# Kernel tuning notes

Hardware: AMD Instinct MI355X
Metric: run time of the kernel (lower is better)

The kernel has to match this reference:

```python
import jax, jax.numpy as jnp
import numpy as np

# Model constants (match init_kwargs)
DIM = 256
H = 8
HD = DIM // H          # 32
WIN = 5                # spatial window_size
QS = 4                 # quant_size
CQS = 2 * QS           # color_quant_size = 8
CWIN = 2               # color_windowsize
W = 64                 # voxels per window (equal-size windows for the reference)
L_XYZ = WIN * QS       # 20 -> table length 40
L_RGB = CWIN * CQS     # 16 -> table length 32


def setup_inputs() -> dict:
    key = jax.random.key(0)
    ks = jax.random.split(key, 12)
    N = 8192
    feats = jax.random.normal(ks[0], (N, DIM), dtype=jnp.float32)
    xyz = jax.random.uniform(ks[1], (N, 3), dtype=jnp.float32) * WIN    # [0, window_size)
    rgb = jax.random.uniform(ks[2], (N, 3), dtype=jnp.float32) * CWIN   # [0, color_windowsize)
    n_coords = jnp.concatenate([xyz, rgb], axis=1)
    std = 0.02
    xyz_shape = (3, 2 * L_XYZ, H, HD)
    rgb_shape = (3, 2 * L_RGB, H, HD)
    return {
        "feats": feats,
        "n_coords": n_coords,
        "qkv_w": jax.random.normal(ks[3], (3 * DIM, DIM), dtype=jnp.float32) * std,
        "qkv_b": jnp.zeros((3 * DIM,), dtype=jnp.float32),
        "q_xyz_t": jax.random.normal(ks[4], xyz_shape, dtype=jnp.float32) * std,
        "k_xyz_t": jax.random.normal(ks[5], xyz_shape, dtype=jnp.float32) * std,
        "v_xyz_t": jax.random.normal(ks[6], xyz_shape, dtype=jnp.float32) * std,
        "q_rgb_t": jax.random.normal(ks[7], rgb_shape, dtype=jnp.float32) * std,
        "k_rgb_t": jax.random.normal(ks[8], rgb_shape, dtype=jnp.float32) * std,
        "v_rgb_t": jax.random.normal(ks[9], rgb_shape, dtype=jnp.float32) * std,
        "proj_w": jax.random.normal(ks[10], (DIM, DIM), dtype=jnp.float32) * std,
        "proj_b": jnp.zeros((DIM,), dtype=jnp.float32),
    }


def _attn_bias(q, k, idx, q_table, k_table):
    """Relative-signal bias added to QK logits.
    q,k: [nw, W, H, hd]; idx: [nw, W, W, 3] int; tables: [3, T, H, hd].
    bias[n,h,i,j] = sum_c q[n,i,h]. q_table[c, idx[n,i,j,c], h] + k[n,j,h]. k_table[c, idx, h]
    Returns (bias [nw,H,W,W], one_hot [nw,W,W,3,T]) so the one-hot is reused for the value bias.
    """
    T = q_table.shape[1]
    oh = jax.nn.one_hot(idx, T, dtype=q.dtype)                # [nw,W,W,3,T]
    dq = jnp.einsum('nihd,cthd->nicht', q, q_table)           # per-voxel dot vs all table rows
    dk = jnp.einsum('njhd,cthd->njcht', k, k_table)
    bias_q = jnp.einsum('nicht,nijct->nhij', dq, oh)
    bias_k = jnp.einsum('njcht,nijct->nhij', dk, oh)
    return bias_q + bias_k, oh


def _value_bias(attn, oh, v_table):
    """out[n,i,h,:] += sum_j attn[n,h,i,j] * sum_c v_table[c, idx[n,i,j,c], h, :]"""
    at = jnp.einsum('nhij,nijct->nhict', attn, oh)            # scatter attn mass onto table rows
    return jnp.einsum('nhict,cthd->nihd', at, v_table)


def reference(feats, n_coords, qkv_w, qkv_b, q_xyz_t, k_xyz_t, v_xyz_t,
              q_rgb_t, k_rgb_t, v_rgb_t, proj_w, proj_b):
    N = feats.shape[0]
    nw = N // W
    scale = HD ** (-0.5)

    # QKV projection, split into per-window heads
    qkv = (feats @ qkv_w.T + qkv_b).reshape(nw, W, 3, H, HD)
    q = qkv[:, :, 0] * scale
    k = qkv[:, :, 1]
    v = qkv[:, :, 2]

    # Quantized relative-signal indices (coordinate deltas, offset to [0, 2L))
    scaled = jnp.concatenate(
        [n_coords[:, 0:3] * QS, n_coords[:, 3:6] * CQS], axis=1)   # [N, 6]
    cw = scaled.reshape(nw, W, 6)
    delta = jnp.floor(cw[:, :, None, :] - cw[:, None, :, :]).astype(jnp.int32)
    offs = jnp.array([L_XYZ] * 3 + [L_RGB] * 3, dtype=jnp.int32)
    hi = jnp.array([2 * L_XYZ - 1] * 3 + [2 * L_RGB - 1] * 3, dtype=jnp.int32)
    idx = jnp.clip(delta + offs, 0, hi)                        # [nw, W, W, 6]
    idx_xyz, idx_rgb = idx[..., :3], idx[..., 3:]

    bias_x, oh_x = _attn_bias(q, k, idx_xyz, q_xyz_t, k_xyz_t)
    bias_r, oh_r = _attn_bias(q, k, idx_rgb, q_rgb_t, k_rgb_t)

    logits = jnp.einsum('nihd,njhd->nhij', q, k) + bias_x + bias_r
    attn = jax.nn.softmax(logits, axis=-1)

    out = (jnp.einsum('nhij,njhd->nihd', attn, v)
           + _value_bias(attn, oh_x, v_xyz_t)
           + _value_bias(attn, oh_r, v_rgb_t))
    out = out.reshape(N, DIM)
    return out @ proj_w.T + proj_b
```

## Files before the change

kernel.cpp:

```cpp
#include <hip/hip_runtime.h>


typedef __attribute__((ext_vector_type(8))) short short8;
typedef __attribute__((ext_vector_type(4))) float f32x4;

__device__ __forceinline__ unsigned short f2bf(float f) {
    union { float f; unsigned int u; } v; v.f = f;
    unsigned int r = v.u + 0x7FFFu + ((v.u >> 16) & 1u);
    return (unsigned short)(r >> 16);
}

#define LFENCE() asm volatile("s_waitcnt lgkmcnt(0)" ::: "memory")

__global__ __launch_bounds__(256) void k_cast(
    const float* __restrict__ feats, const float* __restrict__ qkvw,
    const float* __restrict__ pw,
    ushort* __restrict__ fb, ushort* __restrict__ qwb, ushort* __restrict__ pwb)
{
    int t = blockIdx.x * 256 + threadIdx.x;
    const float* src; ushort* dst; int off;
    if (t < 262144)            { src = feats; dst = fb;  off = t; }
    else if (t < 286720)       { src = qkvw;  dst = qwb; off = t - 262144; }
    else                       { src = pw;    dst = pwb; off = t - 286720; }
    const float* s = src + (size_t)off * 8;
    float4 v0 = *(const float4*)s, v1 = *(const float4*)(s + 4);
    union { ushort u[8]; uint4 v; } pk;
    pk.u[0] = f2bf(v0.x); pk.u[1] = f2bf(v0.y); pk.u[2] = f2bf(v0.z); pk.u[3] = f2bf(v0.w);
    pk.u[4] = f2bf(v1.x); pk.u[5] = f2bf(v1.y); pk.u[6] = f2bf(v1.z); pk.u[7] = f2bf(v1.w);
    *(uint4*)(dst + (size_t)off * 8) = pk.v;
}

__global__ __launch_bounds__(256) void k_qkv(
    const ushort* __restrict__ A, const ushort* __restrict__ B,
    const float* __restrict__ bias,
    ushort* __restrict__ qb, ushort* __restrict__ kb, ushort* __restrict__ vb)
{
    __shared__ __align__(16) ushort a_s[64 * 72];
    __shared__ __align__(16) ushort b_s[64 * 72];
    const int tid = threadIdx.x;
    const int m0 = blockIdx.y * 64;
    const int n0 = blockIdx.x * 64;
    const int w = tid >> 6, wm = w >> 1, wn = w & 1;
    const int l4 = tid & 15, quad = (tid >> 4) & 3;
    f32x4 acc[2][2];
#pragma unroll
    for (int mt = 0; mt < 2; ++mt)
#pragma unroll
        for (int nt = 0; nt < 2; ++nt) acc[mt][nt] = (f32x4){0.f, 0.f, 0.f, 0.f};

    for (int k0 = 0; k0 < 256; k0 += 64) {
#pragma unroll
        for (int l = 0; l < 2; ++l) {
            int e = tid + l * 256;
            int row = e >> 3, kq = e & 7;
            *(uint4*)&a_s[row * 72 + kq * 8] =
                *(const uint4*)(A + (size_t)(m0 + row) * 256 + k0 + kq * 8);
            *(uint4*)&b_s[row * 72 + kq * 8] =
                *(const uint4*)(B + (size_t)(n0 + row) * 256 + k0 + kq * 8);
        }
        __syncthreads();
#pragma unroll
        for (int kh = 0; kh < 2; ++kh) {
            short8 bf0 = *(const short8*)&b_s[(wn * 32 + l4) * 72 + kh * 32 + quad * 8];
            short8 bf1 = *(const short8*)&b_s[(wn * 32 + 16 + l4) * 72 + kh * 32 + quad * 8];
#pragma unroll
            for (int mt = 0; mt < 2; ++mt) {
                short8 af = *(const short8*)&a_s[(wm * 32 + mt * 16 + l4) * 72 + kh * 32 + quad * 8];
                acc[mt][0] = __builtin_amdgcn_mfma_f32_16x16x32_bf16(af, bf0, acc[mt][0], 0, 0, 0);
                acc[mt][1] = __builtin_amdgcn_mfma_f32_16x16x32_bf16(af, bf1, acc[mt][1], 0, 0, 0);
            }
        }
        __syncthreads();
    }
#pragma unroll
    for (int nt = 0; nt < 2; ++nt) {
        int c = n0 + wn * 32 + nt * 16 + l4;
        float bv = bias[c];
        int s = c >> 8, rem = c & 255, h = rem >> 5, d = rem & 31;
        ushort* dst = (s == 0) ? qb : ((s == 1) ? kb : vb);
        float mul = (s == 0) ? 0.17677669529663687f : 1.0f;
#pragma unroll
        for (int mt = 0; mt < 2; ++mt) {
            int mbase = m0 + wm * 32 + mt * 16 + quad * 4;
#pragma unroll
            for (int reg = 0; reg < 4; ++reg) {
                int m = mbase + reg;
                int nw = m >> 6, ii = m & 63;
                dst[((size_t)((nw * 8 + h) * 64 + ii)) * 32 + d] = f2bf((acc[mt][nt][reg] + bv) * mul);
            }
        }
    }
}

#define DBS 44
#define FXS 16777216.0f
#define FXI (1.0f / 16777216.0f)

__global__ __launch_bounds__(256, 2) void k_bias(
    const ushort* __restrict__ qb, const ushort* __restrict__ kb,
    const float* __restrict__ nco,
    const float* __restrict__ kxt, const float* __restrict__ krt,
    float* __restrict__ lgt)
{
    __shared__ __align__(16) float dbuf[64 * DBS];
    __shared__ __align__(16) ushort q_s[64 * 40];
    __shared__ __align__(16) ushort k_s[64 * 40];
    __shared__ __align__(16) ushort tbl[128 * 40];
    __shared__ __align__(16) float cwf[64 * 6];

    const int tid = threadIdx.x;
    const int n = blockIdx.x >> 3;
    const int h = blockIdx.x & 7;
    const int w = tid >> 6;
    const int l4 = tid & 15;
    const int quad = (tid >> 4) & 3;

    const size_t base = (size_t)((n * 8 + h) * 64) * 32;

    {
        int row = tid >> 2, part = tid & 3;
        *(uint4*)&q_s[row * 40 + part * 8] = *(const uint4*)(qb + base + tid * 8);
        *(uint4*)&k_s[row * 40 + part * 8] = *(const uint4*)(kb + base + tid * 8);
    }
    if (tid < 64) {
        const float* cp = nco + (size_t)(n * 64 + tid) * 6;
        cwf[tid * 6 + 0] = cp[0] * 4.f; cwf[tid * 6 + 1] = cp[1] * 4.f;
        cwf[tid * 6 + 2] = cp[2] * 4.f; cwf[tid * 6 + 3] = cp[3] * 8.f;
        cwf[tid * 6 + 4] = cp[4] * 8.f; cwf[tid * 6 + 5] = cp[5] * 8.f;
    }

    auto stageTbl = [&](const float* tbg, int R, int Rpad) {
        for (int e = tid; e < R * 4; e += 256) {
            int r = e >> 2, part = e & 3;
            const float* src = tbg + (size_t)r * 256 + part * 8;
            float4 f0 = *(const float4*)src, f1 = *(const float4*)(src + 4);
            union { ushort u[8]; uint4 v; } pk;
            pk.u[0] = f2bf(f0.x); pk.u[1] = f2bf(f0.y); pk.u[2] = f2bf(f0.z); pk.u[3] = f2bf(f0.w);
            pk.u[4] = f2bf(f1.x); pk.u[5] = f2bf(f1.y); pk.u[6] = f2bf(f1.z); pk.u[7] = f2bf(f1.w);
            *(uint4*)&tbl[r * 40 + part * 8] = pk.v;
        }
        for (int e = tid; e < (Rpad - R) * 40; e += 256) tbl[R * 40 + e] = 0;
    };

    float lg[4][4];
    int ibase[4];
#pragma unroll
    for (int r = 0; r < 4; ++r) ibase[r] = (w * 16 + quad * 4 + r) * DBS;

    auto tgemmC = [&](const ushort* a_s, int c, int T) {
        short8 af = *(const short8*)&a_s[(w * 16 + l4) * 40 + quad * 8];
        const int NT = (T == 40) ? 3 : 2;
        for (int tt = 0; tt < NT; ++tt) {
            short8 bf = *(const short8*)&tbl[(c * T + tt * 16 + l4) * 40 + quad * 8];
            f32x4 a = {0.f, 0.f, 0.f, 0.f};
            a = __builtin_amdgcn_mfma_f32_16x16x32_bf16(af, bf, a, 0, 0, 0);
            int col = tt * 16 + l4;
            int rb = w * 16 + quad * 4;
            if (col < T) {
                dbuf[(rb + 0) * DBS + col] = a[0];
                dbuf[(rb + 1) * DBS + col] = a[1];
                dbuf[(rb + 2) * DBS + col] = a[2];
                dbuf[(rb + 3) * DBS + col] = a[3];
            }
        }
    };

    stageTbl(kxt + h * 32, 120, 128);
    __syncthreads();

    unsigned idxp[24];
    {
        float co[4][6], cl[4][6];
#pragma unroll
        for (int r = 0; r < 4; ++r) {
            int j = w * 16 + quad * 4 + r;
#pragma unroll
            for (int c6 = 0; c6 < 6; ++c6) co[r][c6] = cwf[j * 6 + c6];
        }
#pragma unroll
        for (int tt = 0; tt < 4; ++tt) {
            int i = tt * 16 + l4;
#pragma unroll
            for (int c6 = 0; c6 < 6; ++c6) cl[tt][c6] = cwf[i * 6 + c6];
        }
#pragma unroll
        for (int c6 = 0; c6 < 6; ++c6) {
            const int off = (c6 < 3) ? 20 : 16, hi = (c6 < 3) ? 39 : 31;
#pragma unroll
            for (int tt = 0; tt < 4; ++tt) {
                unsigned p = 0;
#pragma unroll
                for (int r = 0; r < 4; ++r) {
                    int x = min(max((int)floorf(cl[tt][c6] - co[r][c6]) + off, 0), hi);
                    p |= (unsigned)x << (8 * r);
                }
                idxp[c6 * 4 + tt] = p;
            }
        }
    }

    auto gatherT = [&](int cc) {
#pragma unroll
        for (int tt = 0; tt < 4; ++tt) {
            unsigned p = idxp[cc * 4 + tt];
#pragma unroll
            for (int r = 0; r < 4; ++r) {
                int x = (p >> (8 * r)) & 255;
                lg[tt][r] += dbuf[ibase[r] + x];
            }
        }
    };

    {
        short8 ak = *(const short8*)&k_s[(w * 16 + l4) * 40 + quad * 8];
#pragma unroll
        for (int tt = 0; tt < 4; ++tt) {
            short8 bq = *(const short8*)&q_s[(tt * 16 + l4) * 40 + quad * 8];
            f32x4 r = {0.f, 0.f, 0.f, 0.f};
            r = __builtin_amdgcn_mfma_f32_16x16x32_bf16(ak, bq, r, 0, 0, 0);
            lg[tt][0] = r[0]; lg[tt][1] = r[1]; lg[tt][2] = r[2]; lg[tt][3] = r[3];
        }
    }

    tgemmC(k_s, 0, 40); LFENCE();
    gatherT(0); LFENCE();
    tgemmC(k_s, 1, 40); LFENCE();
    gatherT(1); LFENCE();
    tgemmC(k_s, 2, 40); LFENCE();
    gatherT(2);
    __syncthreads();
    stageTbl(krt + h * 32, 96, 96);
    __syncthreads();
    tgemmC(k_s, 0, 32); LFENCE();
    gatherT(3); LFENCE();
    tgemmC(k_s, 1, 32); LFENCE();
    gatherT(4); LFENCE();
    tgemmC(k_s, 2, 32); LFENCE();
    gatherT(5);

    {
        float* lp = lgt + (size_t)(n * 8 + h) * 4096;
#pragma unroll
        for (int tt = 0; tt < 4; ++tt)
#pragma unroll
            for (int reg = 0; reg < 4; ++reg)
                lp[(w * 16 + quad * 4 + reg) * 64 + tt * 16 + l4] = lg[tt][reg];
    }
}

__global__ __launch_bounds__(256, 2) void k_av(
    const ushort* __restrict__ qb, const ushort* __restrict__ vb,
    const float* __restrict__ nco,
    const float* __restrict__ qxt, const float* __restrict__ vxt,
    const float* __restrict__ qrt, const float* __restrict__ vrt,
    const float* __restrict__ lgt,
    ushort* __restrict__ aout)
{
    __shared__ __align__(16) float dbuf[64 * DBS];
    __shared__ __align__(16) ushort U[11264];
    __shared__ __align__(16) float cwf[64 * 6];
    ushort* q_s  = U;
    ushort* tbl  = U + 2560;
    ushort* attn_s = U;
    ushort* v_t    = U + 4608;
    ushort* vtbl   = U + 6912;

    const int tid = threadIdx.x;
    const int n = blockIdx.x >> 3;
    const int h = blockIdx.x & 7;
    const int w = tid >> 6;
    const int lane = tid & 63;
    const int l4 = tid & 15;
    const int quad = (tid >> 4) & 3;

    const size_t base = (size_t)((n * 8 + h) * 64) * 32;

    {
        int row = tid >> 2, part = tid & 3;
        *(uint4*)&q_s[row * 40 + part * 8] = *(const uint4*)(qb + base + tid * 8);
    }
    if (tid < 64) {
        const float* cp = nco + (size_t)(n * 64 + tid) * 6;
        cwf[tid * 6 + 0] = cp[0] * 4.f; cwf[tid * 6 + 1] = cp[1] * 4.f;
        cwf[tid * 6 + 2] = cp[2] * 4.f; cwf[tid * 6 + 3] = cp[3] * 8.f;
        cwf[tid * 6 + 4] = cp[4] * 8.f; cwf[tid * 6 + 5] = cp[5] * 8.f;
    }

    auto stageTbl = [&](const float* tbg, int R, int Rpad) {
        for (int e = tid; e < R * 4; e += 256) {
            int r = e >> 2, part = e & 3;
            const float* src = tbg + (size_t)r * 256 + part * 8;
            float4 f0 = *(const float4*)src, f1 = *(const float4*)(src + 4);
            union { ushort u[8]; uint4 v; } pk;
            pk.u[0] = f2bf(f0.x); pk.u[1] = f2bf(f0.y); pk.u[2] = f2bf(f0.z); pk.u[3] = f2bf(f0.w);
            pk.u[4] = f2bf(f1.x); pk.u[5] = f2bf(f1.y); pk.u[6] = f2bf(f1.z); pk.u[7] = f2bf(f1.w);
            *(uint4*)&tbl[r * 40 + part * 8] = pk.v;
        }
        for (int e = tid; e < (Rpad - R) * 40; e += 256) tbl[R * 40 + e] = 0;
    };
    auto stageVtbl = [&](const float* tbg, int R) {
        for (int e = tid; e < R * 4; e += 256) {
            int r = e >> 2, part = e & 3;
            const float* src = tbg + (size_t)r * 256 + part * 8;
            float4 f0 = *(const float4*)src, f1 = *(const float4*)(src + 4);
            int d0 = part * 8;
            vtbl[(d0 + 0) * 136 + r] = f2bf(f0.x);
            vtbl[(d0 + 1) * 136 + r] = f2bf(f0.y);
            vtbl[(d0 + 2) * 136 + r] = f2bf(f0.z);
            vtbl[(d0 + 3) * 136 + r] = f2bf(f0.w);
            vtbl[(d0 + 4) * 136 + r] = f2bf(f1.x);
            vtbl[(d0 + 5) * 136 + r] = f2bf(f1.y);
            vtbl[(d0 + 6) * 136 + r] = f2bf(f1.z);
            vtbl[(d0 + 7) * 136 + r] = f2bf(f1.w);
        }
    };
    auto stageVt = [&]() {
        int j = tid >> 2, d0 = (tid & 3) * 8;
        uint4 pk = *(const uint4*)(vb + base + tid * 8);
        const ushort* u = (const ushort*)&pk;
#pragma unroll
        for (int ii = 0; ii < 8; ++ii) v_t[(d0 + ii) * 72 + j] = u[ii];
    };

    float lg[4][4];
    {
        const float* lp = lgt + (size_t)(n * 8 + h) * 4096;
        int i0 = w * 16 + quad * 4;
#pragma unroll
        for (int tt = 0; tt < 4; ++tt) {
            f32x4 v = *(const f32x4*)(lp + (size_t)(tt * 16 + l4) * 64 + i0);
            lg[tt][0] = v[0]; lg[tt][1] = v[1]; lg[tt][2] = v[2]; lg[tt][3] = v[3];
        }
    }

    int ibase[4];
#pragma unroll
    for (int r = 0; r < 4; ++r) ibase[r] = (w * 16 + quad * 4 + r) * DBS;

    auto tgemmC = [&](const ushort* a_s, int c, int T) {
        short8 af = *(const short8*)&a_s[(w * 16 + l4) * 40 + quad * 8];
        const int NT = (T == 40) ? 3 : 2;
        for (int tt = 0; tt < NT; ++tt) {
            short8 bf = *(const short8*)&tbl[(c * T + tt * 16 + l4) * 40 + quad * 8];
            f32x4 a = {0.f, 0.f, 0.f, 0.f};
            a = __builtin_amdgcn_mfma_f32_16x16x32_bf16(af, bf, a, 0, 0, 0);
            int col = tt * 16 + l4;
            int rb = w * 16 + quad * 4;
            if (col < T) {
                dbuf[(rb + 0) * DBS + col] = a[0];
                dbuf[(rb + 1) * DBS + col] = a[1];
                dbuf[(rb + 2) * DBS + col] = a[2];
                dbuf[(rb + 3) * DBS + col] = a[3];
            }
        }
    };
    auto zeroOwn = [&]() {
        float4 z = {0.f, 0.f, 0.f, 0.f};
        float4* rb = (float4*)&dbuf[w * 16 * DBS];
        for (int v = lane; v < 176; v += 64) rb[v] = z;
    };

    stageTbl(qxt + h * 32, 120, 128);
    __syncthreads();

    unsigned idxp[24];
    {
        float co[4][6], cl[4][6];
#pragma unroll
        for (int r = 0; r < 4; ++r) {
            int i = w * 16 + quad * 4 + r;
#pragma unroll
            for (int c6 = 0; c6 < 6; ++c6) co[r][c6] = cwf[i * 6 + c6];
        }
#pragma unroll
        for (int tt = 0; tt < 4; ++tt) {
            int j = tt * 16 + l4;
#pragma unroll
            for (int c6 = 0; c6 < 6; ++c6) cl[tt][c6] = cwf[j * 6 + c6];
        }
#pragma unroll
        for (int c6 = 0; c6 < 6; ++c6) {
            const int off = (c6 < 3) ? 20 : 16, hi = (c6 < 3) ? 39 : 31;
#pragma unroll
            for (int tt = 0; tt < 4; ++tt) {
                unsigned p = 0;
#pragma unroll
                for (int r = 0; r < 4; ++r) {
                    int x = min(max((int)floorf(co[r][c6] - cl[tt][c6]) + off, 0), hi);
                    p |= (unsigned)x << (8 * r);
                }
                idxp[c6 * 4 + tt] = p;
            }
        }
    }

    auto gatherC = [&](int cc) {
#pragma unroll
        for (int tt = 0; tt < 4; ++tt) {
            unsigned p = idxp[cc * 4 + tt];
#pragma unroll
            for (int r = 0; r < 4; ++r) {
                int x = (p >> (8 * r)) & 255;
                lg[tt][r] += dbuf[ibase[r] + x];
            }
        }
    };
    auto scatterC = [&](int cc) {
        unsigned* bb = (unsigned*)dbuf;
#pragma unroll
        for (int tt = 0; tt < 4; ++tt) {
            unsigned p = idxp[cc * 4 + tt];
#pragma unroll
            for (int r = 0; r < 4; ++r) {
                int x = (p >> (8 * r)) & 255;
                unsigned q = (unsigned)(lg[tt][r] * FXS + 0.5f);
                atomicAdd(&bb[ibase[r] + x], q);
            }
        }
    };

    tgemmC(q_s, 0, 40); LFENCE();
    gatherC(0); LFENCE();
    tgemmC(q_s, 1, 40); LFENCE();
    gatherC(1); LFENCE();
    tgemmC(q_s, 2, 40);
    __syncthreads();
    gatherC(2);
    stageTbl(qrt + h * 32, 96, 96);
    __syncthreads();
    tgemmC(q_s, 0, 32); LFENCE();
    gatherC(3); LFENCE();
    tgemmC(q_s, 1, 32); LFENCE();
    gatherC(4); LFENCE();
    tgemmC(q_s, 2, 32);
    __syncthreads();
    gatherC(5);
    stageVtbl(vxt + h * 32, 120);
    stageVt();
    __syncthreads();

#pragma unroll
    for (int reg = 0; reg < 4; ++reg) {
        float m = fmaxf(fmaxf(lg[0][reg], lg[1][reg]), fmaxf(lg[2][reg], lg[3][reg]));
        m = fmaxf(m, __shfl_xor(m, 1));
        m = fmaxf(m, __shfl_xor(m, 2));
        m = fmaxf(m, __shfl_xor(m, 4));
        m = fmaxf(m, __shfl_xor(m, 8));
        float s = 0.f;
#pragma unroll
        for (int tt = 0; tt < 4; ++tt) { lg[tt][reg] = __expf(lg[tt][reg] - m); s += lg[tt][reg]; }
        s += __shfl_xor(s, 1); s += __shfl_xor(s, 2);
        s += __shfl_xor(s, 4); s += __shfl_xor(s, 8);
        float inv = 1.f / s;
#pragma unroll
        for (int tt = 0; tt < 4; ++tt) lg[tt][reg] *= inv;
    }
#pragma unroll
    for (int tt = 0; tt < 4; ++tt)
#pragma unroll
        for (int reg = 0; reg < 4; ++reg)
            attn_s[(w * 16 + quad * 4 + reg) * 72 + tt * 16 + l4] = f2bf(lg[tt][reg]);
    zeroOwn();
    __syncthreads();

    f32x4 acc0 = {0.f, 0.f, 0.f, 0.f}, acc1 = {0.f, 0.f, 0.f, 0.f};
#pragma unroll
    for (int s = 0; s < 2; ++s) {
        short8 af = *(const short8*)&attn_s[(w * 16 + l4) * 72 + s * 32 + quad * 8];
        short8 b0 = *(const short8*)&v_t[l4 * 72 + s * 32 + quad * 8];
        short8 b1 = *(const short8*)&v_t[(16 + l4) * 72 + s * 32 + quad * 8];
        acc0 = __builtin_amdgcn_mfma_f32_16x16x32_bf16(af, b0, acc0, 0, 0, 0);
        acc1 = __builtin_amdgcn_mfma_f32_16x16x32_bf16(af, b1, acc1, 0, 0, 0);
    }

    auto atgemmC = [&](int c, int T, int S) {
#pragma unroll
        for (int s = 0; s < S; ++s) {
            int koff = s * 32 + quad * 8;
            short8 af = {0, 0, 0, 0, 0, 0, 0, 0};
            int kr = 0;
            if (koff < T) {
                const unsigned* ap = (const unsigned*)&dbuf[(w * 16 + l4) * DBS + koff];
                uint4 u0 = *(const uint4*)ap;
                uint4 u1 = *(const uint4*)(ap + 4);
                af[0] = (short)f2bf((float)u0.x * FXI); af[1] = (short)f2bf((float)u0.y * FXI);
                af[2] = (short)f2bf((float)u0.z * FXI); af[3] = (short)f2bf((float)u0.w * FXI);
                af[4] = (short)f2bf((float)u1.x * FXI); af[5] = (short)f2bf((float)u1.y * FXI);
                af[6] = (short)f2bf((float)u1.z * FXI); af[7] = (short)f2bf((float)u1.w * FXI);
                kr = c * T + koff;
            }
            short8 b0 = *(const short8*)&vtbl[l4 * 136 + kr];
            short8 b1 = *(const short8*)&vtbl[(16 + l4) * 136 + kr];
            acc0 = __builtin_amdgcn_mfma_f32_16x16x32_bf16(af, b0, acc0, 0, 0, 0);
            acc1 = __builtin_amdgcn_mfma_f32_16x16x32_bf16(af, b1, acc1, 0, 0, 0);
        }
    };

    scatterC(0); LFENCE();
    atgemmC(0, 40, 2); LFENCE();
    zeroOwn(); LFENCE();
    scatterC(1); LFENCE();
    atgemmC(1, 40, 2); LFENCE();
    zeroOwn(); LFENCE();
    scatterC(2); LFENCE();
    atgemmC(2, 40, 2);
    __syncthreads();
    zeroOwn();
    stageVtbl(vrt + h * 32, 96);
    __syncthreads();

    scatterC(3); LFENCE();
    atgemmC(0, 32, 1); LFENCE();
    zeroOwn(); LFENCE();
    scatterC(4); LFENCE();
    atgemmC(1, 32, 1); LFENCE();
    zeroOwn(); LFENCE();
    scatterC(5); LFENCE();
    atgemmC(2, 32, 1);

    {
        ushort* op = aout + (size_t)(n * 64 + w * 16 + quad * 4) * 256 + h * 32;
#pragma unroll
        for (int reg = 0; reg < 4; ++reg) {
            op[reg * 256 + l4] = f2bf(acc0[reg]);
            op[reg * 256 + 16 + l4] = f2bf(acc1[reg]);
        }
    }
}

__global__ __launch_bounds__(256) void k_proj(
    const ushort* __restrict__ A, const ushort* __restrict__ B,
    const float* __restrict__ bias, float* __restrict__ out)
{
    __shared__ __align__(16) ushort a_s[64 * 72];
    __shared__ __align__(16) ushort b_s[64 * 72];
    const int tid = threadIdx.x;
    const int m0 = blockIdx.y * 64;
    const int n0 = blockIdx.x * 64;
    const int w = tid >> 6, wm = w >> 1, wn = w & 1;
    const int l4 = tid & 15, quad = (tid >> 4) & 3;
    f32x4 acc[2][2];
#pragma unroll
    for (int mt = 0; mt < 2; ++mt)
#pragma unroll
        for (int nt = 0; nt < 2; ++nt) acc[mt][nt] = (f32x4){0.f, 0.f, 0.f, 0.f};

    for (int k0 = 0; k0 < 256; k0 += 64) {
#pragma unroll
        for (int l = 0; l < 2; ++l) {
            int e = tid + l * 256;
            int row = e >> 3, kq = e & 7;
            *(uint4*)&a_s[row * 72 + kq * 8] =
                *(const uint4*)(A + (size_t)(m0 + row) * 256 + k0 + kq * 8);
            *(uint4*)&b_s[row * 72 + kq * 8] =
                *(const uint4*)(B + (size_t)(n0 + row) * 256 + k0 + kq * 8);
        }
        __syncthreads();
#pragma unroll
        for (int kh = 0; kh < 2; ++kh) {
            short8 bf0 = *(const short8*)&b_s[(wn * 32 + l4) * 72 + kh * 32 + quad * 8];
            short8 bf1 = *(const short8*)&b_s[(wn * 32 + 16 + l4) * 72 + kh * 32 + quad * 8];
#pragma unroll
            for (int mt = 0; mt < 2; ++mt) {
                short8 af = *(const short8*)&a_s[(wm * 32 + mt * 16 + l4) * 72 + kh * 32 + quad * 8];
                acc[mt][0] = __builtin_amdgcn_mfma_f32_16x16x32_bf16(af, bf0, acc[mt][0], 0, 0, 0);
                acc[mt][1] = __builtin_amdgcn_mfma_f32_16x16x32_bf16(af, bf1, acc[mt][1], 0, 0, 0);
            }
        }
        __syncthreads();
    }
#pragma unroll
    for (int nt = 0; nt < 2; ++nt) {
        int c = n0 + wn * 32 + nt * 16 + l4;
        float bv = bias[c];
#pragma unroll
        for (int mt = 0; mt < 2; ++mt) {
            int mbase = m0 + wm * 32 + mt * 16 + quad * 4;
#pragma unroll
            for (int reg = 0; reg < 4; ++reg)
                out[(size_t)(mbase + reg) * 256 + c] = acc[mt][nt][reg] + bv;
        }
    }
}

extern "C" void kernel_launch(void* const* d_in, const int* in_sizes, int n_in,
                              void* d_out, int out_size, void* d_ws, size_t ws_size,
                              hipStream_t stream)
{
    const float* feats = (const float*)d_in[0];
    const float* nco   = (const float*)d_in[1];
    const float* qkvw  = (const float*)d_in[2];
    const float* qkvb  = (const float*)d_in[3];
    const float* qxt   = (const float*)d_in[4];
    const float* kxt   = (const float*)d_in[5];
    const float* vxt   = (const float*)d_in[6];
    const float* qrt   = (const float*)d_in[7];
    const float* krt   = (const float*)d_in[8];
    const float* vrt   = (const float*)d_in[9];
    const float* pw    = (const float*)d_in[10];
    const float* pb    = (const float*)d_in[11];
    float* out = (float*)d_out;

    ushort* qb  = (ushort*)d_ws;
    ushort* kb  = qb + (size_t)2097152;
    ushort* vb  = kb + (size_t)2097152;
    ushort* aob = vb + (size_t)2097152;
    float*  lgt = (float*)(aob + (size_t)2097152);
    ushort* fb  = (ushort*)(lgt + (size_t)4194304);
    ushort* qwb = fb + (size_t)2097152;
    ushort* pwb = qwb + (size_t)196608;

    k_cast<<<dim3(1152), 256, 0, stream>>>(feats, qkvw, pw, fb, qwb, pwb);
    k_qkv<<<dim3(12, 128), 256, 0, stream>>>(fb, qwb, qkvb, qb, kb, vb);
    k_bias<<<dim3(1024), 256, 0, stream>>>(qb, kb, nco, kxt, krt, lgt);
    k_av<<<dim3(1024), 256, 0, stream>>>(qb, vb, nco, qxt, vxt, qrt, vrt, lgt, aob);
    k_proj<<<dim3(4, 128), 256, 0, stream>>>(aob, pwb, pb, out);
}
```

Before: 149.1 us.

## Batch three coordinate channels per LDS pass in k_av to cut fences

In k_av the per-row delta buffer grows from one channel (44 floats) to three channels (132 floats). The Q-table GEMM, gather, atomic scatter and A·vtable GEMM now each process all three xyz or rgb channels in one pass instead of three passes separated by LDS fences and zeroing. The index-packing loops in both k_bias and k_av are restructured to load coordinates per channel, which lowers register pressure. In exchange the dbuf shared array triples in size, which may reduce how many blocks fit per CU under the (256,2) launch bounds, and each zeroing pass covers three times as much memory.

```diff
diff --git a/kernel.cpp b/kernel.cpp
--- a/kernel.cpp
+++ b/kernel.cpp
@@ -93,6 +93,7 @@
 }
 
 #define DBS 44
+#define SL3 132
 #define FXS 16777216.0f
 #define FXI (1.0f / 16777216.0f)
 
@@ -169,33 +170,21 @@
     __syncthreads();
 
     unsigned idxp[24];
-    {
-        float co[4][6], cl[4][6];
-#pragma unroll
-        for (int r = 0; r < 4; ++r) {
-            int j = w * 16 + quad * 4 + r;
-#pragma unroll
-            for (int c6 = 0; c6 < 6; ++c6) co[r][c6] = cwf[j * 6 + c6];
-        }
+#pragma unroll
+    for (int c6 = 0; c6 < 6; ++c6) {
+        const int off = (c6 < 3) ? 20 : 16, hi = (c6 < 3) ? 39 : 31;
+        float co0 = cwf[(w * 16 + quad * 4 + 0) * 6 + c6];
+        float co1 = cwf[(w * 16 + quad * 4 + 1) * 6 + c6];
+        float co2 = cwf[(w * 16 + quad * 4 + 2) * 6 + c6];
+        float co3 = cwf[(w * 16 + quad * 4 + 3) * 6 + c6];
 #pragma unroll
         for (int tt = 0; tt < 4; ++tt) {
-            int i = tt * 16 + l4;
-#pragma unroll
-            for (int c6 = 0; c6 < 6; ++c6) cl[tt][c6] = cwf[i * 6 + c6];
-        }
-#pragma unroll
-        for (int c6 = 0; c6 < 6; ++c6) {
-            const int off = (c6 < 3) ? 20 : 16, hi = (c6 < 3) ? 39 : 31;
-#pragma unroll
-            for (int tt = 0; tt < 4; ++tt) {
-                unsigned p = 0;
-#pragma unroll
-                for (int r = 0; r < 4; ++r) {
-                    int x = min(max((int)floorf(cl[tt][c6] - co[r][c6]) + off, 0), hi);
-                    p |= (unsigned)x << (8 * r);
-                }
-                idxp[c6 * 4 + tt] = p;
-            }
+            float ci = cwf[(tt * 16 + l4) * 6 + c6];
+            unsigned p = (unsigned)min(max((int)floorf(ci - co0) + off, 0), hi);
+            p |= (unsigned)min(max((int)floorf(ci - co1) + off, 0), hi) << 8;
+            p |= (unsigned)min(max((int)floorf(ci - co2) + off, 0), hi) << 16;
+            p |= (unsigned)min(max((int)floorf(ci - co3) + off, 0), hi) << 24;
+            idxp[c6 * 4 + tt] = p;
         }
     }
 
@@ -256,7 +245,7 @@
     const float* __restrict__ lgt,
     ushort* __restrict__ aout)
 {
-    __shared__ __align__(16) float dbuf[64 * DBS];
+    __shared__ __align__(16) float dbuf[64 * SL3];
     __shared__ __align__(16) ushort U[11264];
     __shared__ __align__(16) float cwf[64 * 6];
     ushort* q_s  = U;
@@ -335,106 +324,96 @@
 
     int ibase[4];
 #pragma unroll
-    for (int r = 0; r < 4; ++r) ibase[r] = (w * 16 + quad * 4 + r) * DBS;
-
-    auto tgemmC = [&](const ushort* a_s, int c, int T) {
-        short8 af = *(const short8*)&a_s[(w * 16 + l4) * 40 + quad * 8];
+    for (int r = 0; r < 4; ++r) ibase[r] = (w * 16 + quad * 4 + r) * SL3;
+
+    auto tgemm3 = [&](int T) {
+        short8 af = *(const short8*)&q_s[(w * 16 + l4) * 40 + quad * 8];
         const int NT = (T == 40) ? 3 : 2;
-        for (int tt = 0; tt < NT; ++tt) {
-            short8 bf = *(const short8*)&tbl[(c * T + tt * 16 + l4) * 40 + quad * 8];
-            f32x4 a = {0.f, 0.f, 0.f, 0.f};
-            a = __builtin_amdgcn_mfma_f32_16x16x32_bf16(af, bf, a, 0, 0, 0);
-            int col = tt * 16 + l4;
-            int rb = w * 16 + quad * 4;
-            if (col < T) {
-                dbuf[(rb + 0) * DBS + col] = a[0];
-                dbuf[(rb + 1) * DBS + col] = a[1];
-                dbuf[(rb + 2) * DBS + col] = a[2];
-                dbuf[(rb + 3) * DBS + col] = a[3];
-            }
-        }
-    };
-    auto zeroOwn = [&]() {
+        int rb = w * 16 + quad * 4;
+#pragma unroll
+        for (int c = 0; c < 3; ++c) {
+            for (int tt = 0; tt < NT; ++tt) {
+                short8 bf = *(const short8*)&tbl[(c * T + tt * 16 + l4) * 40 + quad * 8];
+                f32x4 a = {0.f, 0.f, 0.f, 0.f};
+                a = __builtin_amdgcn_mfma_f32_16x16x32_bf16(af, bf, a, 0, 0, 0);
+                int col = tt * 16 + l4;
+                if (col < T) {
+                    int sc = c * DBS + col;
+                    dbuf[(rb + 0) * SL3 + sc] = a[0];
+                    dbuf[(rb + 1) * SL3 + sc] = a[1];
+                    dbuf[(rb + 2) * SL3 + sc] = a[2];
+                    dbuf[(rb + 3) * SL3 + sc] = a[3];
+                }
+            }
+        }
+    };
+    auto zeroAll = [&]() {
         float4 z = {0.f, 0.f, 0.f, 0.f};
-        float4* rb = (float4*)&dbuf[w * 16 * DBS];
-        for (int v = lane; v < 176; v += 64) rb[v] = z;
+        float4* rb = (float4*)&dbuf[w * 16 * SL3];
+        for (int v = lane; v < 528; v += 64) rb[v] = z;
     };
 
     stageTbl(qxt + h * 32, 120, 128);
     __syncthreads();
 
     unsigned idxp[24];
-    {
-        float co[4][6], cl[4][6];
-#pragma unroll
-        for (int r = 0; r < 4; ++r) {
-            int i = w * 16 + quad * 4 + r;
-#pragma unroll
-            for (int c6 = 0; c6 < 6; ++c6) co[r][c6] = cwf[i * 6 + c6];
-        }
+#pragma unroll
+    for (int c6 = 0; c6 < 6; ++c6) {
+        const int off = (c6 < 3) ? 20 : 16, hi = (c6 < 3) ? 39 : 31;
+        float co0 = cwf[(w * 16 + quad * 4 + 0) * 6 + c6];
+        float co1 = cwf[(w * 16 + quad * 4 + 1) * 6 + c6];
+        float co2 = cwf[(w * 16 + quad * 4 + 2) * 6 + c6];
+        float co3 = cwf[(w * 16 + quad * 4 + 3) * 6 + c6];
 #pragma unroll
         for (int tt = 0; tt < 4; ++tt) {
-            int j = tt * 16 + l4;
-#pragma unroll
-            for (int c6 = 0; c6 < 6; ++c6) cl[tt][c6] = cwf[j * 6 + c6];
-        }
-#pragma unroll
-        for (int c6 = 0; c6 < 6; ++c6) {
-            const int off = (c6 < 3) ? 20 : 16, hi = (c6 < 3) ? 39 : 31;
+            float cj = cwf[(tt * 16 + l4) * 6 + c6];
+            unsigned p = (unsigned)min(max((int)floorf(co0 - cj) + off, 0), hi);
+            p |= (unsigned)min(max((int)floorf(co1 - cj) + off, 0), hi) << 8;
+            p |= (unsigned)min(max((int)floorf(co2 - cj) + off, 0), hi) << 16;
+            p |= (unsigned)min(max((int)floorf(co3 - cj) + off, 0), hi) << 24;
+            idxp[c6 * 4 + tt] = p;
+        }
+    }
+
+    auto gather3 = [&](int half) {
+#pragma unroll
+        for (int c = 0; c < 3; ++c) {
 #pragma unroll
             for (int tt = 0; tt < 4; ++tt) {
-                unsigned p = 0;
+                unsigned p = idxp[(half * 3 + c) * 4 + tt];
 #pragma unroll
                 for (int r = 0; r < 4; ++r) {
-                    int x = min(max((int)floorf(co[r][c6] - cl[tt][c6]) + off, 0), hi);
-                    p |= (unsigned)x << (8 * r);
+                    int x = (p >> (8 * r)) & 255;
+                    lg[tt][r] += dbuf[ibase[r] + c * DBS + x];
                 }
-                idxp[c6 * 4 + tt] = p;
-            }
-        }
-    }
-
-    auto gatherC = [&](int cc) {
-#pragma unroll
-        for (int tt = 0; tt < 4; ++tt) {
-            unsigned p = idxp[cc * 4 + tt];
-#pragma unroll
-            for (int r = 0; r < 4; ++r) {
-                int x = (p >> (8 * r)) & 255;
-                lg[tt][r] += dbuf[ibase[r] + x];
-            }
-        }
-    };
-    auto scatterC = [&](int cc) {
+            }
+        }
+    };
+    auto scatter3 = [&](int half) {
         unsigned* bb = (unsigned*)dbuf;
 #pragma unroll
-        for (int tt = 0; tt < 4; ++tt) {
-            unsigned p = idxp[cc * 4 + tt];
-#pragma unroll
-            for (int r = 0; r < 4; ++r) {
-                int x = (p >> (8 * r)) & 255;
-                unsigned q = (unsigned)(lg[tt][r] * FXS + 0.5f);
-                atomicAdd(&bb[ibase[r] + x], q);
-            }
-        }
-    };
-
-    tgemmC(q_s, 0, 40); LFENCE();
-    gatherC(0); LFENCE();
-    tgemmC(q_s, 1, 40); LFENCE();
-    gatherC(1); LFENCE();
-    tgemmC(q_s, 2, 40);
-    __syncthreads();
-    gatherC(2);
+        for (int c = 0; c < 3; ++c) {
+#pragma unroll
+            for (int tt = 0; tt < 4; ++tt) {
+                unsigned p = idxp[(half * 3 + c) * 4 + tt];
+#pragma unroll
+                for (int r = 0; r < 4; ++r) {
+                    int x = (p >> (8 * r)) & 255;
+                    unsigned q = (unsigned)(lg[tt][r] * FXS + 0.5f);
+                    atomicAdd(&bb[ibase[r] + c * DBS + x], q);
+                }
+            }
+        }
+    };
+
+    tgemm3(40);
+    __syncthreads();
+    gather3(0);
     stageTbl(qrt + h * 32, 96, 96);
     __syncthreads();
-    tgemmC(q_s, 0, 32); LFENCE();
-    gatherC(3); LFENCE();
-    tgemmC(q_s, 1, 32); LFENCE();
-    gatherC(4); LFENCE();
-    tgemmC(q_s, 2, 32);
-    __syncthreads();
-    gatherC(5);
+    tgemm3(32);
+    __syncthreads();
+    gather3(1);
     stageVtbl(vxt + h * 32, 120);
     stageVt();
     __syncthreads();
@@ -460,7 +439,7 @@
 #pragma unroll
         for (int reg = 0; reg < 4; ++reg)
             attn_s[(w * 16 + quad * 4 + reg) * 72 + tt * 16 + l4] = f2bf(lg[tt][reg]);
-    zeroOwn();
+    zeroAll();
     __syncthreads();
 
     f32x4 acc0 = {0.f, 0.f, 0.f, 0.f}, acc1 = {0.f, 0.f, 0.f, 0.f};
@@ -473,50 +452,41 @@
         acc1 = __builtin_amdgcn_mfma_f32_16x16x32_bf16(af, b1, acc1, 0, 0, 0);
     }
 
-    auto atgemmC = [&](int c, int T, int S) {
-#pragma unroll
-        for (int s = 0; s < S; ++s) {
-            int koff = s * 32 + quad * 8;
-            short8 af = {0, 0, 0, 0, 0, 0, 0, 0};
-            int kr = 0;
-            if (koff < T) {
-                const unsigned* ap = (const unsigned*)&dbuf[(w * 16 + l4) * DBS + koff];
-                uint4 u0 = *(const uint4*)ap;
-                uint4 u1 = *(const uint4*)(ap + 4);
-                af[0] = (short)f2bf((float)u0.x * FXI); af[1] = (short)f2bf((float)u0.y * FXI);
-                af[2] = (short)f2bf((float)u0.z * FXI); af[3] = (short)f2bf((float)u0.w * FXI);
-                af[4] = (short)f2bf((float)u1.x * FXI); af[5] = (short)f2bf((float)u1.y * FXI);
-                af[6] = (short)f2bf((float)u1.z * FXI); af[7] = (short)f2bf((float)u1.w * FXI);
-                kr = c * T + koff;
-            }
-            short8 b0 = *(const short8*)&vtbl[l4 * 136 + kr];
-            short8 b1 = *(const short8*)&vtbl[(16 + l4) * 136 + kr];
-            acc0 = __builtin_amdgcn_mfma_f32_16x16x32_bf16(af, b0, acc0, 0, 0, 0);
-            acc1 = __builtin_amdgcn_mfma_f32_16x16x32_bf16(af, b1, acc1, 0, 0, 0);
-        }
-    };
-
-    scatterC(0); LFENCE();
-    atgemmC(0, 40, 2); LFENCE();
-    zeroOwn(); LFENCE();
-    scatterC(1); LFENCE();
-    atgemmC(1, 40, 2); LFENCE();
-    zeroOwn(); LFENCE();
-    scatterC(2); LFENCE();
-    atgemmC(2, 40, 2);
-    __syncthreads();
-    zeroOwn();
+    auto atgemm3 = [&](int T, int S) {
+        int rowb = (w * 16 + l4) * SL3;
+#pragma unroll
+        for (int c = 0; c < 3; ++c) {
+#pragma unroll
+            for (int s = 0; s < S; ++s) {
+                int koff = s * 32 + quad * 8;
+                short8 af = {0, 0, 0, 0, 0, 0, 0, 0};
+                int kr = 0;
+                if (koff < T) {
+                    const unsigned* ap = (const unsigned*)&dbuf[rowb + c * DBS + koff];
+                    uint4 u0 = *(const uint4*)ap;
+                    uint4 u1 = *(const uint4*)(ap + 4);
+                    af[0] = (short)f2bf((float)u0.x * FXI); af[1] = (short)f2bf((float)u0.y * FXI);
+                    af[2] = (short)f2bf((float)u0.z * FXI); af[3] = (short)f2bf((float)u0.w * FXI);
+                    af[4] = (short)f2bf((float)u1.x * FXI); af[5] = (short)f2bf((float)u1.y * FXI);
+                    af[6] = (short)f2bf((float)u1.z * FXI); af[7] = (short)f2bf((float)u1.w * FXI);
+                    kr = c * T + koff;
+                }
+                short8 b0 = *(const short8*)&vtbl[l4 * 136 + kr];
+                short8 b1 = *(const short8*)&vtbl[(16 + l4) * 136 + kr];
+                acc0 = __builtin_amdgcn_mfma_f32_16x16x32_bf16(af, b0, acc0, 0, 0, 0);
+                acc1 = __builtin_amdgcn_mfma_f32_16x16x32_bf16(af, b1, acc1, 0, 0, 0);
+            }
+        }
+    };
+
+    scatter3(0); LFENCE();
+    atgemm3(40, 2);
+    __syncthreads();
+    zeroAll();
     stageVtbl(vrt + h * 32, 96);
     __syncthreads();
-
-    scatterC(3); LFENCE();
-    atgemmC(0, 32, 1); LFENCE();
-    zeroOwn(); LFENCE();
-    scatterC(4); LFENCE();
-    atgemmC(1, 32, 1); LFENCE();
-    zeroOwn(); LFENCE();
-    scatterC(5); LFENCE();
-    atgemmC(2, 32, 1);
+    scatter3(1); LFENCE();
+    atgemm3(32, 1);
 
     {
         ushort* op = aout + (size_t)(n * 64 + w * 16 + quad * 4) * 256 + h * 32;
```

Result: no change. 148.4 us (median of 2 runs) (-0.5%).
